# Optimization experiments

Hardware: AMD Instinct MI355X
Metric: run time of the kernel (lower is better)

Reference implementation:

```python
import jax, jax.numpy as jnp
import numpy as np

B, IN_DIM, CTRL, N_LOC, LOC_SZ, OUT = 2048, 512, 512, 65536, 64, 1
EPS = 1e-8


def setup_inputs() -> dict:
    key = jax.random.key(0)
    ks = jax.random.split(key, 11)
    s = 0.02
    return {
        "x": jax.random.normal(ks[0], (B, IN_DIM), dtype=jnp.float32),
        # Controller: h = tanh(x W_h + b_h), gate = x W_g + b_g
        "W_h": jax.random.normal(ks[1], (IN_DIM, CTRL), dtype=jnp.float32) * s,
        "b_h": jnp.zeros((CTRL,), dtype=jnp.float32),
        "W_g": jax.random.normal(ks[2], (IN_DIM, 1), dtype=jnp.float32) * s,
        "b_g": jnp.zeros((1,), dtype=jnp.float32),
        # Head read-key net: key = tanh(h W_k + b_k)
        "W_k": jax.random.normal(ks[3], (CTRL, LOC_SZ), dtype=jnp.float32) * s,
        "b_k": jnp.zeros((LOC_SZ,), dtype=jnp.float32),
        # Memory matrix [locations, location_size]
        "M": jax.random.normal(ks[4], (N_LOC, LOC_SZ), dtype=jnp.float32),
        # Output linear: (ctrl_dim + location_size) -> output_dim
        "W_out": jax.random.normal(ks[5], (CTRL + LOC_SZ, OUT), dtype=jnp.float32) * s,
        "b_out": jnp.zeros((OUT,), dtype=jnp.float32),
    }


def reference(x, W_h, b_h, W_g, b_g, W_k, b_k, M, W_out, b_out):
    # Vectorized version of the original per-sample Python loop.
    h = jnp.tanh(x @ W_h + b_h)                # [B, ctrl_dim]
    gate = x @ W_g + b_g                       # [B, 1]
    read_key = jnp.tanh(h @ W_k + b_k)         # [B, loc_sz]
    # Cosine-similarity content addressing over memory rows.
    kn = read_key / (jnp.linalg.norm(read_key, axis=-1, keepdims=True) + EPS)
    Mn = M / (jnp.linalg.norm(M, axis=-1, keepdims=True) + EPS)
    sim = kn @ Mn.T                            # [B, locations]
    w_read = jax.nn.softmax(sim, axis=-1)      # [B, locations]
    r = w_read @ M                             # [B, loc_sz]
    feat = jnp.concatenate([h, r], axis=-1)    # [B, ctrl_dim + loc_sz]
    output = (feat @ W_out + b_out)[:, 0]      # [B]
    # Original returns last-iteration h, gate, w_read alongside output.
    return output, h[-1], gate[-1], w_read[-1]
```

## Files before the change

kernel.cpp:

```cpp
#include <hip/hip_runtime.h>

#define B_SZ 2048
#define IN_DIM 512
#define CTRL 512
#define N_LOC 65536
#define NSPLIT 64
#define LPS (N_LOC / NSPLIT)
#define EPSV 1e-8f
#define LOG2E 1.4426950408889634f

typedef __attribute__((ext_vector_type(8))) short bf16x8;
typedef __attribute__((ext_vector_type(4))) float f32x4;
typedef __attribute__((ext_vector_type(16))) float f32x16;
typedef __attribute__((ext_vector_type(4))) unsigned int u32x4;
typedef __attribute__((ext_vector_type(8))) unsigned short u16x8;

static __device__ __forceinline__ unsigned int cvtpk(float lo, float hi) {
  unsigned int r;
  asm("v_cvt_pk_bf16_f32 %0, %1, %2" : "=v"(r) : "v"(lo), "v"(hi));
  return r;
}
static __device__ __forceinline__ unsigned short f2bf_hw(float f) {
  return (unsigned short)(cvtpk(f, f) & 0xffffu);
}
static __device__ __forceinline__ float bf2f(unsigned short u) {
  return __builtin_bit_cast(float, ((unsigned int)u) << 16);
}
static __device__ __forceinline__ float exp2_fast(float x) {
  float r;
  asm("v_exp_f32 %0, %1" : "=v"(r) : "v"(x));
  return r;
}

__global__ __launch_bounds__(256) void k_prep_all(const float* __restrict__ x,
                                                  const float* __restrict__ Wh,
                                                  const float* __restrict__ Wk,
                                                  const float* __restrict__ M,
                                                  unsigned short* __restrict__ xb,
                                                  unsigned short* __restrict__ Wht,
                                                  unsigned short* __restrict__ Wkt,
                                                  unsigned short* __restrict__ Mn_t,
                                                  unsigned short* __restrict__ Mt_t) {
  const int bx = blockIdx.x, t = threadIdx.x;
  if (bx < 512) {
    const int base = bx * 2048 + t * 8;
    const float4 a = *(const float4*)&x[base];
    const float4 b = *(const float4*)&x[base + 4];
    u16x8 o;
    unsigned int u0 = cvtpk(a.x, a.y), u1 = cvtpk(a.z, a.w);
    unsigned int u2 = cvtpk(b.x, b.y), u3 = cvtpk(b.z, b.w);
    o[0] = (unsigned short)u0; o[1] = (unsigned short)(u0 >> 16);
    o[2] = (unsigned short)u1; o[3] = (unsigned short)(u1 >> 16);
    o[4] = (unsigned short)u2; o[5] = (unsigned short)(u2 >> 16);
    o[6] = (unsigned short)u3; o[7] = (unsigned short)(u3 >> 16);
    *(u16x8*)&xb[base] = o;
  } else if (bx < 584) {
    __shared__ float ld[64][65];
    const bool isWh = bx < 576;
    const int id = isWh ? bx - 512 : bx - 576;
    const int ti = isWh ? (id >> 3) : id;
    const int tj = isWh ? (id & 7) : 0;
    const int ncol = isWh ? CTRL : 64;
    const float* src = isWh ? Wh : Wk;
#pragma unroll
    for (int i = 0; i < 4; i++) {
      const int c = t + i * 256;
      const int r = c >> 4, c4 = (c & 15) * 4;
      const float4 v = *(const float4*)&src[(size_t)(ti * 64 + r) * ncol + tj * 64 + c4];
      ld[r][c4] = v.x; ld[r][c4 + 1] = v.y; ld[r][c4 + 2] = v.z; ld[r][c4 + 3] = v.w;
    }
    __syncthreads();
    unsigned short* dst = isWh ? Wht : Wkt;
#pragma unroll
    for (int i = 0; i < 2; i++) {
      const int c = t + i * 256;
      const int col = c >> 3, k8 = (c & 7) * 8;
      u16x8 o;
#pragma unroll
      for (int j = 0; j < 4; j++) {
        unsigned int u = cvtpk(ld[k8 + 2 * j][col], ld[k8 + 2 * j + 1][col]);
        o[2 * j] = (unsigned short)u;
        o[2 * j + 1] = (unsigned short)(u >> 16);
      }
      *(u16x8*)&dst[(size_t)(tj * 64 + col) * IN_DIM + ti * 64 + k8] = o;
    }
  } else {
    const int b = bx - 584;
    const int c4 = t & 15, lg = t >> 4;
    float vv[4][4], ss[4];
#pragma unroll
    for (int r = 0; r < 4; r++) {
      const int loc = b * 64 + lg * 4 + r;
      const float4 f = *(const float4*)&M[(size_t)loc * 64 + c4 * 4];
      vv[r][0] = f.x; vv[r][1] = f.y; vv[r][2] = f.z; vv[r][3] = f.w;
      ss[r] = f.x * f.x + f.y * f.y + f.z * f.z + f.w * f.w;
    }
#pragma unroll
    for (int r = 0; r < 4; r++)
#pragma unroll
      for (int off = 1; off < 16; off <<= 1) ss[r] += __shfl_xor(ss[r], off);
#pragma unroll
    for (int r = 0; r < 4; r++) {
      const float s = (1.f / (sqrtf(ss[r]) + EPSV)) * LOG2E;
      uint2 u;
      u.x = cvtpk(vv[r][0] * s, vv[r][1] * s);
      u.y = cvtpk(vv[r][2] * s, vv[r][3] * s);
      *(uint2*)&Mn_t[(size_t)b * 4096 + (lg * 4 + r) * 64 + c4 * 4] = u;
    }
#pragma unroll
    for (int j = 0; j < 4; j++) {
      uint2 u;
      u.x = cvtpk(vv[0][j], vv[1][j]);
      u.y = cvtpk(vv[2][j], vv[3][j]);
      *(uint2*)&Mt_t[(size_t)b * 4096 + (c4 * 4 + j) * 64 + lg * 4] = u;
    }
  }
}

__global__ __launch_bounds__(256) void k_hgemm(const unsigned short* __restrict__ xb,
                                               const unsigned short* __restrict__ Wht,
                                               const float* __restrict__ bh,
                                               float* __restrict__ h) {
  __shared__ __align__(16) unsigned short xs[64 * 32];
  __shared__ __align__(16) unsigned short wsb[64 * 32];
  const int t = threadIdx.x, lane = t & 63, w = t >> 6, lo = lane & 15, g = lane >> 4;
  const int bm = blockIdx.x * 64, bn = blockIdx.y * 64;
  f32x4 acc[4];
#pragma unroll
  for (int rt = 0; rt < 4; rt++) acc[rt] = (f32x4){0.f, 0.f, 0.f, 0.f};

  for (int k0 = 0; k0 < IN_DIM; k0 += 32) {
    {
      const int r = t >> 2, k8 = (t & 3) * 8;
      *(u16x8*)&xs[r * 32 + (k8 ^ ((r & 3) * 8))] =
          *(const u16x8*)&xb[(size_t)(bm + r) * IN_DIM + k0 + k8];
      *(u16x8*)&wsb[r * 32 + (k8 ^ ((r & 3) * 8))] =
          *(const u16x8*)&Wht[(size_t)(bn + r) * IN_DIM + k0 + k8];
    }
    __syncthreads();
    const int koff = (8 * g) ^ ((lo & 3) * 8);
    const bf16x8 bfr = *(const bf16x8*)&wsb[(16 * w + lo) * 32 + koff];
#pragma unroll
    for (int rt = 0; rt < 4; rt++) {
      const bf16x8 afr = *(const bf16x8*)&xs[(16 * rt + lo) * 32 + koff];
      acc[rt] = __builtin_amdgcn_mfma_f32_16x16x32_bf16(afr, bfr, acc[rt], 0, 0, 0);
    }
    __syncthreads();
  }
  const int col = bn + 16 * w + lo;
  const float b = bh[col];
#pragma unroll
  for (int rt = 0; rt < 4; rt++)
#pragma unroll
    for (int q = 0; q < 4; q++) {
      const int row = bm + 16 * rt + 4 * g + q;
      h[(size_t)row * CTRL + col] = tanhf(acc[rt][q] + b);
    }
}

__global__ __launch_bounds__(256) void k_readkey(const float* __restrict__ h_,
                                                 const unsigned short* __restrict__ Wkt,
                                                 const float* __restrict__ bk,
                                                 const float* __restrict__ x,
                                                 const float* __restrict__ Wg,
                                                 const float* __restrict__ bg,
                                                 unsigned short* __restrict__ kn_bf,
                                                 float* __restrict__ out) {
  __shared__ float sAcc[4][32][65];
  __shared__ float red[4];
  const int t = threadIdx.x, lane = t & 63, w = t >> 6;
  const int l31 = lane & 31, hh = lane >> 5;
  if (blockIdx.x < 64) {
    const int row0 = blockIdx.x * 32;
    f32x16 acc[2];
    acc[0] = (f32x16)(0.f); acc[1] = (f32x16)(0.f);
#pragma unroll
    for (int kk = 0; kk < 8; kk++) {
      const int kb = 128 * w + 16 * kk + 8 * hh;
      const float4 a0 = *(const float4*)&h_[(size_t)(row0 + l31) * CTRL + kb];
      const float4 a1 = *(const float4*)&h_[(size_t)(row0 + l31) * CTRL + kb + 4];
      const u32x4 av = {cvtpk(a0.x, a0.y), cvtpk(a0.z, a0.w), cvtpk(a1.x, a1.y), cvtpk(a1.z, a1.w)};
      const bf16x8 afr = __builtin_bit_cast(bf16x8, av);
#pragma unroll
      for (int ct = 0; ct < 2; ct++) {
        const bf16x8 bfr = *(const bf16x8*)&Wkt[(size_t)(32 * ct + l31) * IN_DIM + kb];
        acc[ct] = __builtin_amdgcn_mfma_f32_32x32x16_bf16(afr, bfr, acc[ct], 0, 0, 0);
      }
    }
#pragma unroll
    for (int ct = 0; ct < 2; ct++)
#pragma unroll
      for (int r = 0; r < 16; r++)
        sAcc[w][(r & 3) + 8 * (r >> 2) + 4 * hh][32 * ct + l31] = acc[ct][r];
    __syncthreads();
    const int row = t >> 3, c8 = (t & 7) * 8;
    float v[8];
    float ss = 0.f;
#pragma unroll
    for (int j = 0; j < 8; j++) {
      const float s = sAcc[0][row][c8 + j] + sAcc[1][row][c8 + j] +
                      sAcc[2][row][c8 + j] + sAcc[3][row][c8 + j] + bk[c8 + j];
      v[j] = tanhf(s);
      ss += v[j] * v[j];
    }
    ss += __shfl_xor(ss, 1);
    ss += __shfl_xor(ss, 2);
    ss += __shfl_xor(ss, 4);
    const float inv = 1.f / (sqrtf(ss) + EPSV);
    u16x8 o;
#pragma unroll
    for (int j = 0; j < 4; j++) {
      const unsigned int u = cvtpk(v[2 * j] * inv, v[2 * j + 1] * inv);
      o[2 * j] = (unsigned short)u;
      o[2 * j + 1] = (unsigned short)(u >> 16);
    }
    *(u16x8*)&kn_bf[(size_t)(row0 + row) * 64 + c8] = o;
  } else {
    out[2048 + t] = h_[(size_t)(B_SZ - 1) * CTRL + t];
    out[2048 + 256 + t] = h_[(size_t)(B_SZ - 1) * CTRL + 256 + t];
    float p = x[(size_t)(B_SZ - 1) * IN_DIM + t] * Wg[t] +
              x[(size_t)(B_SZ - 1) * IN_DIM + 256 + t] * Wg[256 + t];
#pragma unroll
    for (int off = 32; off >= 1; off >>= 1) p += __shfl_xor(p, off);
    if ((t & 63) == 0) red[t >> 6] = p;
    __syncthreads();
    if (t == 0) out[2048 + 512] = red[0] + red[1] + red[2] + red[3] + bg[0];
  }
}

__global__ __launch_bounds__(256, 4) void k_attn(const unsigned short* __restrict__ kn_bf,
                                                 const unsigned short* __restrict__ Mn_t,
                                                 const unsigned short* __restrict__ Mt_t,
                                                 float* __restrict__ l_part,
                                                 unsigned short* __restrict__ r_bf,
                                                 float* __restrict__ wdump) {
  __shared__ __align__(16) unsigned short sMn[2][4096];
  __shared__ __align__(16) unsigned short sMt[2][4096];
  const int sp = blockIdx.x, rb = blockIdx.y;
  const int t = threadIdx.x, lane = t & 63, w = t >> 6;
  const int l31 = lane & 31, hh = lane >> 5, l7 = lane & 7;
  const int row0 = rb * 128 + 32 * w;

  bf16x8 bq[4];
#pragma unroll
  for (int kk = 0; kk < 4; kk++)
    bq[kk] = *(const bf16x8*)&kn_bf[(size_t)(row0 + l31) * 64 + 16 * kk + 8 * hh];

  const int c0 = t, c1 = t + 256;
  const int r0 = c0 >> 3, d0 = r0 * 64 + (((c0 & 7) * 8) ^ ((r0 & 7) * 8));
  const int r1 = c1 >> 3, d1 = r1 * 64 + (((c1 & 7) * 8) ^ ((r1 & 7) * 8));
  {
    const size_t gb = (size_t)(sp * 16) * 4096;
    *(u16x8*)&sMn[0][d0] = *(const u16x8*)&Mn_t[gb + c0 * 8];
    *(u16x8*)&sMn[0][d1] = *(const u16x8*)&Mn_t[gb + c1 * 8];
    *(u16x8*)&sMt[0][d0] = *(const u16x8*)&Mt_t[gb + c0 * 8];
    *(u16x8*)&sMt[0][d1] = *(const u16x8*)&Mt_t[gb + c1 * 8];
  }
  __syncthreads();

  f32x16 Racc[2];
  Racc[0] = (f32x16)(0.f); Racc[1] = (f32x16)(0.f);
  float lrun = 0.f;

  u16x8 rn0, rn1, rt0, rt1;
  for (int it = 0; it < 16; ++it) {
    const int cur = it & 1;
    if (it < 15) {
      const size_t gn = (size_t)(sp * 16 + it + 1) * 4096;
      rn0 = *(const u16x8*)&Mn_t[gn + c0 * 8];
      rn1 = *(const u16x8*)&Mn_t[gn + c1 * 8];
      rt0 = *(const u16x8*)&Mt_t[gn + c0 * 8];
      rt1 = *(const u16x8*)&Mt_t[gn + c1 * 8];
    }

    f32x16 cst[2];
    cst[0] = (f32x16)(0.f); cst[1] = (f32x16)(0.f);
    __builtin_amdgcn_s_setprio(1);
#pragma unroll
    for (int kk = 0; kk < 4; kk++) {
      const int koff = ((2 * kk + hh) ^ l7) * 8;
#pragma unroll
      for (int lt = 0; lt < 2; lt++) {
        const bf16x8 afr = *(const bf16x8*)&sMn[cur][(32 * lt + l31) * 64 + koff];
        cst[lt] = __builtin_amdgcn_mfma_f32_32x32x16_bf16(afr, bq[kk], cst[lt], 0, 0, 0);
      }
    }
    __builtin_amdgcn_s_setprio(0);

#pragma unroll
    for (int lt = 0; lt < 2; lt++)
#pragma unroll
      for (int r = 0; r < 16; r++) {
        const float e = exp2_fast(cst[lt][r]);
        cst[lt][r] = e;
        lrun += e;
      }

    if (rb == 15 && w == 3 && l31 == 31) {
#pragma unroll
      for (int lt = 0; lt < 2; lt++)
#pragma unroll
        for (int rr = 0; rr < 4; rr++)
          *(float4*)&wdump[sp * 1024 + it * 64 + 32 * lt + 8 * rr + 4 * hh] =
              make_float4(cst[lt][4 * rr], cst[lt][4 * rr + 1], cst[lt][4 * rr + 2],
                          cst[lt][4 * rr + 3]);
    }

    unsigned int pk[16];
#pragma unroll
    for (int lt = 0; lt < 2; lt++)
#pragma unroll
      for (int rr = 0; rr < 4; rr++) {
        pk[lt * 8 + rr * 2 + 0] = cvtpk(cst[lt][4 * rr + 0], cst[lt][4 * rr + 1]);
        pk[lt * 8 + rr * 2 + 1] = cvtpk(cst[lt][4 * rr + 2], cst[lt][4 * rr + 3]);
      }

#pragma unroll
    for (int kk = 0; kk < 4; kk++) {
      const int lt = kk >> 1;
      const int rrE = 2 * (kk & 1), rrO = rrE + 1;
      const unsigned int s0 = hh ? pk[lt * 8 + rrE * 2 + 0] : pk[lt * 8 + rrO * 2 + 0];
      const unsigned int s1 = hh ? pk[lt * 8 + rrE * 2 + 1] : pk[lt * 8 + rrO * 2 + 1];
      const unsigned int g0 = (unsigned int)__shfl_xor((int)s0, 32);
      const unsigned int g1 = (unsigned int)__shfl_xor((int)s1, 32);
      u32x4 aw;
      if (hh == 0)
        aw = (u32x4){pk[lt * 8 + rrE * 2 + 0], pk[lt * 8 + rrE * 2 + 1], g0, g1};
      else
        aw = (u32x4){g0, g1, pk[lt * 8 + rrO * 2 + 0], pk[lt * 8 + rrO * 2 + 1]};
      const bf16x8 afr = __builtin_bit_cast(bf16x8, aw);
      const int koff = ((2 * kk + hh) ^ l7) * 8;
      __builtin_amdgcn_s_setprio(1);
#pragma unroll
      for (int dt = 0; dt < 2; dt++) {
        const bf16x8 bfr = *(const bf16x8*)&sMt[cur][(32 * dt + l31) * 64 + koff];
        Racc[dt] = __builtin_amdgcn_mfma_f32_32x32x16_bf16(afr, bfr, Racc[dt], 0, 0, 0);
      }
      __builtin_amdgcn_s_setprio(0);
    }

    if (it < 15) {
      const int nxt = cur ^ 1;
      *(u16x8*)&sMn[nxt][d0] = rn0; *(u16x8*)&sMn[nxt][d1] = rn1;
      *(u16x8*)&sMt[nxt][d0] = rt0; *(u16x8*)&sMt[nxt][d1] = rt1;
    }
    __syncthreads();
  }

  lrun += __shfl_xor(lrun, 32);
  if (hh == 0) l_part[(size_t)(row0 + l31) * NSPLIT + sp] = lrun;

#pragma unroll
  for (int dt = 0; dt < 2; dt++)
#pragma unroll
    for (int r = 0; r < 16; r++) {
      const int brow = (r & 3) + 8 * (r >> 2) + 4 * hh;
      r_bf[((size_t)(row0 + brow) * NSPLIT + sp) * 64 + 32 * dt + l31] = f2bf_hw(Racc[dt][r]);
    }
}

__global__ __launch_bounds__(256) void k_post(const float* __restrict__ l_part,
                                              const unsigned short* __restrict__ r_bf,
                                              const float* __restrict__ h,
                                              const float* __restrict__ Wout,
                                              const float* __restrict__ bout,
                                              const float* __restrict__ wdump,
                                              float* __restrict__ out) {
  const int lane = threadIdx.x & 63, w = threadIdx.x >> 6;
  const int bx = blockIdx.x;
  if (bx < 512) {
    const int row = bx * 4 + w;
    float l = l_part[(size_t)row * NSPLIT + lane];
#pragma unroll
    for (int off = 32; off >= 1; off >>= 1) l += __shfl_xor(l, off);
    float rd = 0.f;
    for (int sp2 = 0; sp2 < NSPLIT; sp2++)
      rd += bf2f(r_bf[((size_t)row * NSPLIT + sp2) * 64 + lane]);
    rd /= l;
    float acc = Wout[CTRL + lane] * rd;
    for (int k = lane; k < CTRL; k += 64) acc += h[(size_t)row * CTRL + k] * Wout[k];
#pragma unroll
    for (int off = 32; off >= 1; off >>= 1) acc += __shfl_xor(acc, off);
    if (lane == 0) out[row] = acc + bout[0];
  } else {
    float l = l_part[(size_t)(B_SZ - 1) * NSPLIT + lane];
#pragma unroll
    for (int off = 32; off >= 1; off >>= 1) l += __shfl_xor(l, off);
    const float rl = 1.f / l;
    const int i = ((bx - 512) * 256 + threadIdx.x) * 4;
    const float4 v = *(const float4*)&wdump[i];
    *(float4*)&out[2048 + 512 + 1 + i] = make_float4(v.x * rl, v.y * rl, v.z * rl, v.w * rl);
  }
}

extern "C" void kernel_launch(void* const* d_in, const int* in_sizes, int n_in,
                              void* d_out, int out_size, void* d_ws, size_t ws_size,
                              hipStream_t stream) {
  const float* x = (const float*)d_in[0];
  const float* Wh = (const float*)d_in[1];
  const float* bh = (const float*)d_in[2];
  const float* Wg = (const float*)d_in[3];
  const float* bg = (const float*)d_in[4];
  const float* Wk = (const float*)d_in[5];
  const float* bk = (const float*)d_in[6];
  const float* M = (const float*)d_in[7];
  const float* Wout = (const float*)d_in[8];
  const float* bout = (const float*)d_in[9];
  float* out = (float*)d_out;

  float* ws = (float*)d_ws;
  float* h = ws;
  float* l_part = h + 1048576;
  float* wdump = l_part + 131072;
  unsigned short* r_bf = (unsigned short*)(wdump + 65536);
  unsigned short* kn_bf = r_bf + 8388608;
  unsigned short* Mn_t = kn_bf + 131072;
  unsigned short* Mt_t = Mn_t + 4194304;
  unsigned short* xb = Mt_t + 4194304;
  unsigned short* Wht = xb + 1048576;
  unsigned short* Wkt = Wht + 262144;

  hipLaunchKernelGGL(k_prep_all, dim3(1608), dim3(256), 0, stream,
                     x, Wh, Wk, M, xb, Wht, Wkt, Mn_t, Mt_t);
  hipLaunchKernelGGL(k_hgemm, dim3(32, 8), dim3(256), 0, stream, xb, Wht, bh, h);
  hipLaunchKernelGGL(k_readkey, dim3(65), dim3(256), 0, stream,
                     h, Wkt, bk, x, Wg, bg, kn_bf, out);
  hipLaunchKernelGGL(k_attn, dim3(NSPLIT, 16), dim3(256), 0, stream,
                     kn_bf, Mn_t, Mt_t, l_part, r_bf, wdump);
  hipLaunchKernelGGL(k_post, dim3(512 + 64), dim3(256), 0, stream,
                     l_part, r_bf, h, Wout, bout, wdump, out);
}
```

Before: 87.49 us.

## Process two 32-row query tiles per wave in attention kernel to reuse LDS memory tiles

Each wave in the attention kernel now handles 64 query rows instead of 32, so every memory-tile fragment read from LDS feeds two MFMAs. The grid is halved along the row dimension, which halves the global traffic for streaming the memory matrix. The cross-half lane exchange uses permlane32_swap in place of shuffles. This raises register pressure (occupancy hint lowered from 4 to 2) and halves the block count, which risks less latency hiding.

```diff
diff --git a/kernel.cpp b/kernel.cpp
--- a/kernel.cpp
+++ b/kernel.cpp
@@ -228,7 +228,7 @@
   }
 }
 
-__global__ __launch_bounds__(256, 4) void k_attn(const unsigned short* __restrict__ kn_bf,
+__global__ __launch_bounds__(256, 2) void k_attn(const unsigned short* __restrict__ kn_bf,
                                                  const unsigned short* __restrict__ Mn_t,
                                                  const unsigned short* __restrict__ Mt_t,
                                                  float* __restrict__ l_part,
@@ -239,12 +239,15 @@
   const int sp = blockIdx.x, rb = blockIdx.y;
   const int t = threadIdx.x, lane = t & 63, w = t >> 6;
   const int l31 = lane & 31, hh = lane >> 5, l7 = lane & 7;
-  const int row0 = rb * 128 + 32 * w;
-
-  bf16x8 bq[4];
-#pragma unroll
-  for (int kk = 0; kk < 4; kk++)
-    bq[kk] = *(const bf16x8*)&kn_bf[(size_t)(row0 + l31) * 64 + 16 * kk + 8 * hh];
+  const int row0 = rb * 256 + 64 * w;
+
+  bf16x8 bq[2][4];
+#pragma unroll
+  for (int rs = 0; rs < 2; rs++)
+#pragma unroll
+    for (int kk = 0; kk < 4; kk++)
+      bq[rs][kk] =
+          *(const bf16x8*)&kn_bf[(size_t)(row0 + 32 * rs + l31) * 64 + 16 * kk + 8 * hh];
 
   const int c0 = t, c1 = t + 256;
   const int r0 = c0 >> 3, d0 = r0 * 64 + (((c0 & 7) * 8) ^ ((r0 & 7) * 8));
@@ -258,9 +261,12 @@
   }
   __syncthreads();
 
-  f32x16 Racc[2];
-  Racc[0] = (f32x16)(0.f); Racc[1] = (f32x16)(0.f);
-  float lrun = 0.f;
+  f32x16 Racc[2][2];
+#pragma unroll
+  for (int rs = 0; rs < 2; rs++)
+#pragma unroll
+    for (int dt = 0; dt < 2; dt++) Racc[rs][dt] = (f32x16)(0.f);
+  float lr0a = 0.f, lr0b = 0.f, lr1a = 0.f, lr1b = 0.f;
 
   u16x8 rn0, rn1, rt0, rt1;
   for (int it = 0; it < 16; ++it) {
@@ -273,68 +279,69 @@
       rt1 = *(const u16x8*)&Mt_t[gn + c1 * 8];
     }
 
-    f32x16 cst[2];
-    cst[0] = (f32x16)(0.f); cst[1] = (f32x16)(0.f);
+    f32x16 cst[2][2];
+#pragma unroll
+    for (int rs = 0; rs < 2; rs++)
+#pragma unroll
+      for (int lt = 0; lt < 2; lt++) cst[rs][lt] = (f32x16)(0.f);
     __builtin_amdgcn_s_setprio(1);
 #pragma unroll
     for (int kk = 0; kk < 4; kk++) {
       const int koff = ((2 * kk + hh) ^ l7) * 8;
-#pragma unroll
-      for (int lt = 0; lt < 2; lt++) {
-        const bf16x8 afr = *(const bf16x8*)&sMn[cur][(32 * lt + l31) * 64 + koff];
-        cst[lt] = __builtin_amdgcn_mfma_f32_32x32x16_bf16(afr, bq[kk], cst[lt], 0, 0, 0);
-      }
+      const bf16x8 a0 = *(const bf16x8*)&sMn[cur][l31 * 64 + koff];
+      const bf16x8 a1 = *(const bf16x8*)&sMn[cur][(32 + l31) * 64 + koff];
+      cst[0][0] = __builtin_amdgcn_mfma_f32_32x32x16_bf16(a0, bq[0][kk], cst[0][0], 0, 0, 0);
+      cst[0][1] = __builtin_amdgcn_mfma_f32_32x32x16_bf16(a1, bq[0][kk], cst[0][1], 0, 0, 0);
+      cst[1][0] = __builtin_amdgcn_mfma_f32_32x32x16_bf16(a0, bq[1][kk], cst[1][0], 0, 0, 0);
+      cst[1][1] = __builtin_amdgcn_mfma_f32_32x32x16_bf16(a1, bq[1][kk], cst[1][1], 0, 0, 0);
     }
     __builtin_amdgcn_s_setprio(0);
 
 #pragma unroll
-    for (int lt = 0; lt < 2; lt++)
-#pragma unroll
-      for (int r = 0; r < 16; r++) {
-        const float e = exp2_fast(cst[lt][r]);
-        cst[lt][r] = e;
-        lrun += e;
-      }
-
-    if (rb == 15 && w == 3 && l31 == 31) {
+    for (int r = 0; r < 16; r++) {
+      cst[0][0][r] = exp2_fast(cst[0][0][r]); lr0a += cst[0][0][r];
+      cst[0][1][r] = exp2_fast(cst[0][1][r]); lr0b += cst[0][1][r];
+      cst[1][0][r] = exp2_fast(cst[1][0][r]); lr1a += cst[1][0][r];
+      cst[1][1][r] = exp2_fast(cst[1][1][r]); lr1b += cst[1][1][r];
+    }
+
+    if (rb == 7 && w == 3 && l31 == 31) {
 #pragma unroll
       for (int lt = 0; lt < 2; lt++)
 #pragma unroll
         for (int rr = 0; rr < 4; rr++)
           *(float4*)&wdump[sp * 1024 + it * 64 + 32 * lt + 8 * rr + 4 * hh] =
-              make_float4(cst[lt][4 * rr], cst[lt][4 * rr + 1], cst[lt][4 * rr + 2],
-                          cst[lt][4 * rr + 3]);
-    }
-
-    unsigned int pk[16];
-#pragma unroll
-    for (int lt = 0; lt < 2; lt++)
-#pragma unroll
-      for (int rr = 0; rr < 4; rr++) {
-        pk[lt * 8 + rr * 2 + 0] = cvtpk(cst[lt][4 * rr + 0], cst[lt][4 * rr + 1]);
-        pk[lt * 8 + rr * 2 + 1] = cvtpk(cst[lt][4 * rr + 2], cst[lt][4 * rr + 3]);
-      }
+              make_float4(cst[1][lt][4 * rr], cst[1][lt][4 * rr + 1], cst[1][lt][4 * rr + 2],
+                          cst[1][lt][4 * rr + 3]);
+    }
+
+    unsigned int pkq[2][2][8];
+#pragma unroll
+    for (int rs = 0; rs < 2; rs++)
+#pragma unroll
+      for (int lt = 0; lt < 2; lt++)
+#pragma unroll
+        for (int m = 0; m < 8; m++)
+          pkq[rs][lt][m] = cvtpk(cst[rs][lt][2 * m], cst[rs][lt][2 * m + 1]);
 
 #pragma unroll
     for (int kk = 0; kk < 4; kk++) {
-      const int lt = kk >> 1;
-      const int rrE = 2 * (kk & 1), rrO = rrE + 1;
-      const unsigned int s0 = hh ? pk[lt * 8 + rrE * 2 + 0] : pk[lt * 8 + rrO * 2 + 0];
-      const unsigned int s1 = hh ? pk[lt * 8 + rrE * 2 + 1] : pk[lt * 8 + rrO * 2 + 1];
-      const unsigned int g0 = (unsigned int)__shfl_xor((int)s0, 32);
-      const unsigned int g1 = (unsigned int)__shfl_xor((int)s1, 32);
-      u32x4 aw;
-      if (hh == 0)
-        aw = (u32x4){pk[lt * 8 + rrE * 2 + 0], pk[lt * 8 + rrE * 2 + 1], g0, g1};
-      else
-        aw = (u32x4){g0, g1, pk[lt * 8 + rrO * 2 + 0], pk[lt * 8 + rrO * 2 + 1]};
-      const bf16x8 afr = __builtin_bit_cast(bf16x8, aw);
+      const int lt = kk >> 1, e4 = (kk & 1) * 4;
       const int koff = ((2 * kk + hh) ^ l7) * 8;
+      const bf16x8 b0f = *(const bf16x8*)&sMt[cur][l31 * 64 + koff];
+      const bf16x8 b1f = *(const bf16x8*)&sMt[cur][(32 + l31) * 64 + koff];
       __builtin_amdgcn_s_setprio(1);
 #pragma unroll
-      for (int dt = 0; dt < 2; dt++) {
-        const bf16x8 bfr = *(const bf16x8*)&sMt[cur][(32 * dt + l31) * 64 + koff];
-        Racc[dt] = __builtin_amdgcn_mfma_f32_32x32x16_bf16(afr, bfr, Racc[dt], 0, 0, 0);
+      for (int rs = 0; rs < 2; rs++) {
+        auto s0 = __builtin_amdgcn_permlane32_swap(pkq[rs][lt][e4 + 2], pkq[rs][lt][e4 + 0],
+                                                   false, false);
+        auto s1 = __builtin_amdgcn_permlane32_swap(pkq[rs][lt][e4 + 3], pkq[rs][lt][e4 + 1],
+                                                   false, false);
+        const u32x4 aw = {(unsigned int)s0[1], (unsigned int)s1[1], (unsigned int)s0[0],
+                          (unsigned int)s1[0]};
+        const bf16x8 afr = __builtin_bit_cast(bf16x8, aw);
+        Racc[rs][0] = __builtin_amdgcn_mfma_f32_32x32x16_bf16(afr, b0f, Racc[rs][0], 0, 0, 0);
+        Racc[rs][1] = __builtin_amdgcn_mfma_f32_32x32x16_bf16(afr, b1f, Racc[rs][1], 0, 0, 0);
       }
       __builtin_amdgcn_s_setprio(0);
     }
@@ -347,16 +354,24 @@
     __syncthreads();
   }
 
-  lrun += __shfl_xor(lrun, 32);
-  if (hh == 0) l_part[(size_t)(row0 + l31) * NSPLIT + sp] = lrun;
-
-#pragma unroll
-  for (int dt = 0; dt < 2; dt++)
-#pragma unroll
-    for (int r = 0; r < 16; r++) {
-      const int brow = (r & 3) + 8 * (r >> 2) + 4 * hh;
-      r_bf[((size_t)(row0 + brow) * NSPLIT + sp) * 64 + 32 * dt + l31] = f2bf_hw(Racc[dt][r]);
-    }
+  float lr0 = lr0a + lr0b, lr1 = lr1a + lr1b;
+  lr0 += __shfl_xor(lr0, 32);
+  lr1 += __shfl_xor(lr1, 32);
+  if (hh == 0) {
+    l_part[(size_t)(row0 + l31) * NSPLIT + sp] = lr0;
+    l_part[(size_t)(row0 + 32 + l31) * NSPLIT + sp] = lr1;
+  }
+
+#pragma unroll
+  for (int rs = 0; rs < 2; rs++)
+#pragma unroll
+    for (int dt = 0; dt < 2; dt++)
+#pragma unroll
+      for (int r = 0; r < 16; r++) {
+        const int brow = (r & 3) + 8 * (r >> 2) + 4 * hh;
+        r_bf[((size_t)(row0 + 32 * rs + brow) * NSPLIT + sp) * 64 + 32 * dt + l31] =
+            f2bf_hw(Racc[rs][dt][r]);
+      }
 }
 
 __global__ __launch_bounds__(256) void k_post(const float* __restrict__ l_part,
@@ -425,7 +440,7 @@
   hipLaunchKernelGGL(k_hgemm, dim3(32, 8), dim3(256), 0, stream, xb, Wht, bh, h);
   hipLaunchKernelGGL(k_readkey, dim3(65), dim3(256), 0, stream,
                      h, Wkt, bk, x, Wg, bg, kn_bf, out);
-  hipLaunchKernelGGL(k_attn, dim3(NSPLIT, 16), dim3(256), 0, stream,
+  hipLaunchKernelGGL(k_attn, dim3(NSPLIT, 8), dim3(256), 0, stream,
                      kn_bf, Mn_t, Mt_t, l_part, r_bf, wdump);
   hipLaunchKernelGGL(k_post, dim3(512 + 64), dim3(256), 0, stream,
                      l_part, r_bf, h, Wout, bout, wdump, out);
```

Result: faster. 79.14 us (-9.5%).
